# Kernel tuning notes

Hardware: AMD Instinct MI355X
Metric: run time of the kernel (lower is better)

## Reference

```python
import jax, jax.numpy as jnp
import numpy as np

DEPTH = 2
EPS = 1e-12

def _l2norm(x, axis=-1):
    n = jnp.sqrt(jnp.sum(x * x, axis=axis, keepdims=True))
    return x / jnp.maximum(n, EPS)

def setup_inputs() -> dict:
    key = jax.random.key(0)
    k1, k2, k3, k4, k5 = jax.random.split(key, 5)
    N, D, R, E = 50000, 100, 1000, 800000
    features = jax.random.normal(k1, (N, D), dtype=jnp.float32)
    rel_emb = jax.random.normal(k2, (R, D), dtype=jnp.float32)
    none_relation = jax.random.normal(k3, (D,), dtype=jnp.float32)
    # edge list sorted by destination row (matches coalesced sparse layout
    # assumed by the original: softmax values align with edge order)
    rows = jnp.sort(jax.random.randint(k4, (E,), 0, N))
    cols = jax.random.randint(k5, (E,), 0, N)
    adj_index = jnp.stack([rows, cols], axis=1).astype(jnp.int64)
    return {"features": features, "rel_emb": rel_emb,
            "adj_index": adj_index, "none_relation": none_relation}

def reference(features, rel_emb, adj_index, none_relation):
    N = features.shape[0]
    rows = adj_index[:, 0]  # destination (softmax segment, scatter target)
    cols = adj_index[:, 1]  # neighbor (gather source)
    feats = jnp.tanh(features)
    outputs = [feats]
    nr = _l2norm(none_relation, axis=0)  # [D]
    for _ in range(DEPTH):
        neighs = feats[cols]                      # [E, D] gather
        score = -jnp.einsum('ed,d->e', _l2norm(neighs), nr)  # [E]
        # sparse softmax over each destination row's edges
        m = jax.ops.segment_max(score, rows, num_segments=N)
        e = jnp.exp(score - m[rows])
        denom = jax.ops.segment_sum(e, rows, num_segments=N)
        att = e / denom[rows]                     # [E]
        new_feats = jax.ops.segment_sum(neighs * att[:, None], rows,
                                        num_segments=N)  # [N, D]
        feats = jnp.tanh(new_feats)
        outputs.append(feats)
    return jnp.concatenate(outputs, axis=1)  # [N, D*(DEPTH+1)]
```

## Files before the change

kernel.cpp:

```cpp
#include <hip/hip_runtime.h>
#include <math.h>

#define D_FEAT 100
#define ROW_STRIDE 300
#define ROWQ 26

__device__ __forceinline__ float fast_tanh(float x) {
    float ax = fabsf(x);
    float e  = __expf(2.f * ax);
    float t  = 1.f - 2.f / (e + 1.f);
    return copysignf(t, x);
}

__device__ __forceinline__ unsigned pack_bf16x2(float a, float b) {
    unsigned ua = __float_as_uint(a);
    unsigned ub = __float_as_uint(b);
    ua += 0x7fffu + ((ua >> 16) & 1u);
    ub += 0x7fffu + ((ub >> 16) & 1u);
    return (ua >> 16) | (ub & 0xffff0000u);
}
__device__ __forceinline__ unsigned long long pack_bf16x4(float a, float b,
                                                          float c, float d) {
    return (unsigned long long)pack_bf16x2(a, b) |
           ((unsigned long long)pack_bf16x2(c, d) << 32);
}
__device__ __forceinline__ void unpack_bf16x4(unsigned long long u,
                                              float& x0, float& x1,
                                              float& x2, float& x3) {
    unsigned lo = (unsigned)u, hi = (unsigned)(u >> 32);
    x0 = __uint_as_float(lo << 16);
    x1 = __uint_as_float(lo & 0xffff0000u);
    x2 = __uint_as_float(hi << 16);
    x3 = __uint_as_float(hi & 0xffff0000u);
}

__device__ __forceinline__ float half_reduce(float v) {
    #pragma unroll
    for (int off = 16; off; off >>= 1) v += __shfl_xor(v, off, 64);
    return v;
}

__global__ __launch_bounds__(256) void tanh_score_kernel(
    const float* __restrict__ features,
    float* __restrict__ out,
    unsigned long long* __restrict__ tab0,
    float* __restrict__ escore0,
    const float* __restrict__ none_rel,
    const int* __restrict__ adj,
    int* __restrict__ startArr,
    int E, int N)
{
    int gtid = blockIdx.x * blockDim.x + threadIdx.x;
    if (gtid <= N) {
        if (gtid == N) startArr[N] = E;
        else {
            int lo = 0, hi = E;
            while (lo < hi) {
                int mid = (lo + hi) >> 1;
                if (adj[2 * mid] < gtid) lo = mid + 1; else hi = mid;
            }
            startArr[gtid] = lo;
        }
    }

    int waveId = gtid >> 6;
    int lane = threadIdx.x & 63;
    int half = lane >> 5;
    int l    = lane & 31;
    int n    = waveId * 2 + half;
    const bool valid_n = (n < N);
    const bool fact = valid_n && (l >= 1) && (l <= 25);

    float x0 = 0.f, x1 = 0.f, x2 = 0.f, x3 = 0.f;
    if (fact) {
        float4 f = ((const float4*)(features + (size_t)n * D_FEAT))[l - 1];
        x0 = fast_tanh(f.x); x1 = fast_tanh(f.y);
        x2 = fast_tanh(f.z); x3 = fast_tanh(f.w);
        ((float4*)(out + (size_t)n * ROW_STRIDE))[l - 1] = make_float4(x0, x1, x2, x3);
        if (tab0) tab0[(size_t)n * ROWQ + l] = pack_bf16x4(x0, x1, x2, x3);
    }

    float nx = 0.f, ny = 0.f, nz = 0.f, nw = 0.f;
    if (l >= 1 && l <= 25) {
        float4 v = ((const float4*)none_rel)[l - 1];
        nx = v.x; ny = v.y; nz = v.z; nw = v.w;
    }
    float ss = half_reduce(nx * nx + ny * ny + nz * nz + nw * nw);
    float inv_nr = 1.f / fmaxf(sqrtf(ss), 1e-12f);

    float dot = half_reduce(x0 * nx + x1 * ny + x2 * nz + x3 * nw) * inv_nr;
    float sq  = half_reduce(x0 * x0 + x1 * x1 + x2 * x2 + x3 * x3);
    if (l == 0 && valid_n) {
        float es = __expf(-dot / fmaxf(sqrtf(sq), 1e-12f));
        if (tab0) tab0[(size_t)n * ROWQ] = (unsigned long long)__float_as_uint(es);
        else      escore0[n] = es;
    }
}

template <bool TAB>
__global__ __launch_bounds__(256) void attn_kernel(
    const void* __restrict__ prev,
    float* __restrict__ outp,
    unsigned long long* __restrict__ tab_out,
    const int2* __restrict__ adj2,
    const int* __restrict__ start,
    const float* __restrict__ escore_in,
    float* __restrict__ escore_out,
    const float* __restrict__ none_rel,
    int N)
{
    int waveId = (int)((blockIdx.x * blockDim.x + threadIdx.x) >> 6);
    int lane = threadIdx.x & 63;
    int half = lane >> 5;
    int l    = lane & 31;
    int n    = waveId * 2 + half;
    const bool valid_n = (n < N);
    const bool fact = valid_n && (l >= 1) && (l <= 25);
    const int base = half << 5;

    int e0 = 0, e1 = 0;
    if (valid_n) { e0 = start[n]; e1 = start[n + 1]; }
    const int deg = e1 - e0;

    int   c0 = 0, c1 = 0;
    float w0 = 0.f, w1 = 0.f;
    if (l < deg)      { c0 = adj2[e0 + l].y;      if (!TAB) w0 = escore_in[c0]; }
    if (l + 32 < deg) { c1 = adj2[e0 + l + 32].y; if (!TAB) w1 = escore_in[c1]; }

    int maxdeg = deg;
    { int o = __shfl_xor(maxdeg, 32, 64); maxdeg = maxdeg > o ? maxdeg : o; }

    const unsigned long long* tab = (const unsigned long long*)prev;
    const float* pf32 = (const float*)prev;

    float d_acc = 0.f, a0 = 0.f, a1 = 0.f, a2 = 0.f, a3 = 0.f;
    const int cap1 = maxdeg < 32 ? maxdeg : 32;
    for (int r = 0; r < cap1; r += 8) {
        #pragma unroll
        for (int j = 0; j < 8; ++j) {
            int   i = r + j;
            int   c = __shfl(c0, base + i, 64);
            float w, p0, p1, p2, p3;
            if (TAB) {
                bool on = valid_n && (i < deg) && (l <= 25);
                unsigned long long v = 0;
                if (on) v = tab[(size_t)(unsigned)(c * ROWQ + l)];
                w = __shfl(__uint_as_float((unsigned)v), base, 64);
                unpack_bf16x4(v, p0, p1, p2, p3);
            } else {
                w = __shfl(w0, base + i, 64);
                p0 = p1 = p2 = p3 = 0.f;
                if (fact && (i < deg)) {
                    float4 v = ((const float4*)(pf32 + (size_t)c * ROW_STRIDE))[l - 1];
                    p0 = v.x; p1 = v.y; p2 = v.z; p3 = v.w;
                }
            }
            d_acc += w;
            a0 += w * p0; a1 += w * p1; a2 += w * p2; a3 += w * p3;
        }
    }
    const int cap2 = maxdeg < 64 ? maxdeg : 64;
    for (int r = 32; r < cap2; r += 8) {
        #pragma unroll
        for (int j = 0; j < 8; ++j) {
            int   i = r + j;
            int   c = __shfl(c1, base + i - 32, 64);
            float w, p0, p1, p2, p3;
            if (TAB) {
                bool on = valid_n && (i < deg) && (l <= 25);
                unsigned long long v = 0;
                if (on) v = tab[(size_t)(unsigned)(c * ROWQ + l)];
                w = __shfl(__uint_as_float((unsigned)v), base, 64);
                unpack_bf16x4(v, p0, p1, p2, p3);
            } else {
                w = __shfl(w1, base + i - 32, 64);
                p0 = p1 = p2 = p3 = 0.f;
                if (fact && (i < deg)) {
                    float4 v = ((const float4*)(pf32 + (size_t)c * ROW_STRIDE))[l - 1];
                    p0 = v.x; p1 = v.y; p2 = v.z; p3 = v.w;
                }
            }
            d_acc += w;
            a0 += w * p0; a1 += w * p1; a2 += w * p2; a3 += w * p3;
        }
    }
    for (int e = e0 + 64; e < e1; ++e) {
        int c = adj2[e].y;
        float w, p0, p1, p2, p3;
        if (TAB) {
            unsigned long long v = 0;
            if (l <= 25) v = tab[(size_t)(unsigned)(c * ROWQ + l)];
            w = __shfl(__uint_as_float((unsigned)v), base, 64);
            unpack_bf16x4(v, p0, p1, p2, p3);
        } else {
            w = escore_in[c];
            p0 = p1 = p2 = p3 = 0.f;
            if (fact) {
                float4 v = ((const float4*)(pf32 + (size_t)c * ROW_STRIDE))[l - 1];
                p0 = v.x; p1 = v.y; p2 = v.z; p3 = v.w;
            }
        }
        d_acc += w;
        a0 += w * p0; a1 += w * p1; a2 += w * p2; a3 += w * p3;
    }

    const float inv_d = (deg > 0) ? 1.f / d_acc : 0.f;
    float r0 = fast_tanh(a0 * inv_d);
    float r1 = fast_tanh(a1 * inv_d);
    float r2 = fast_tanh(a2 * inv_d);
    float r3 = fast_tanh(a3 * inv_d);
    if (fact) {
        ((float4*)(outp + (size_t)n * ROW_STRIDE))[l - 1] = make_float4(r0, r1, r2, r3);
        if (TAB && tab_out)
            tab_out[(size_t)n * ROWQ + l] = pack_bf16x4(r0, r1, r2, r3);
    } else {
        r0 = r1 = r2 = r3 = 0.f;
    }

    if (tab_out || escore_out) {
        float nx = 0.f, ny = 0.f, nz = 0.f, nw = 0.f;
        if (l >= 1 && l <= 25) {
            float4 v = ((const float4*)none_rel)[l - 1];
            nx = v.x; ny = v.y; nz = v.z; nw = v.w;
        }
        float ss = half_reduce(nx * nx + ny * ny + nz * nz + nw * nw);
        float inv_nr = 1.f / fmaxf(sqrtf(ss), 1e-12f);
        float dot = half_reduce(r0 * nx + r1 * ny + r2 * nz + r3 * nw) * inv_nr;
        float sq  = half_reduce(r0 * r0 + r1 * r1 + r2 * r2 + r3 * r3);
        if (l == 0 && valid_n) {
            float es = __expf(-dot / fmaxf(sqrtf(sq), 1e-12f));
            if (TAB) tab_out[(size_t)n * ROWQ] = (unsigned long long)__float_as_uint(es);
            else     escore_out[n] = es;
        }
    }
}

extern "C" void kernel_launch(void* const* d_in, const int* in_sizes, int n_in,
                              void* d_out, int out_size, void* d_ws, size_t ws_size,
                              hipStream_t stream) {
    const float* features = (const float*)d_in[0];
    const int*   adj      = (const int*)d_in[2];
    const float* none_rel = (const float*)d_in[3];
    float* out = (float*)d_out;

    const int N = in_sizes[0] / D_FEAT;
    const int E = in_sizes[2] / 2;

    size_t off = 0;
    auto take = [&](size_t bytes) { size_t o = off; off = (off + bytes + 15) & ~(size_t)15; return o; };
    char* w = (char*)d_ws;
    int*   start   = (int*)  (w + take(sizeof(int)   * (size_t)(N + 1)));
    float* escore0 = (float*)(w + take(sizeof(float) * (size_t)N));
    float* escore1 = (float*)(w + take(sizeof(float) * (size_t)N));
    size_t tab_off0 = take(sizeof(unsigned long long) * (size_t)N * ROWQ);
    size_t tab_off1 = take(sizeof(unsigned long long) * (size_t)N * ROWQ);
    const bool use_tab = (ws_size >= off);
    unsigned long long* tab0 = use_tab ? (unsigned long long*)(w + tab_off0) : nullptr;
    unsigned long long* tab1 = use_tab ? (unsigned long long*)(w + tab_off1) : nullptr;

    const int pairs = (N + 1) / 2;
    const int node_blocks = (pairs * 64 + 255) / 256;
    const int2* adj2 = (const int2*)adj;

    tanh_score_kernel<<<node_blocks, 256, 0, stream>>>(features, out, tab0,
                                                       escore0, none_rel,
                                                       adj, start, E, N);
    if (use_tab) {
        attn_kernel<true><<<node_blocks, 256, 0, stream>>>(
            tab0, out + D_FEAT, tab1, adj2, start, nullptr, nullptr, none_rel, N);
        attn_kernel<true><<<node_blocks, 256, 0, stream>>>(
            tab1, out + 2 * D_FEAT, nullptr, adj2, start, nullptr, nullptr, none_rel, N);
    } else {
        attn_kernel<false><<<node_blocks, 256, 0, stream>>>(
            out, out + D_FEAT, nullptr, adj2, start, escore0, escore1, none_rel, N);
        attn_kernel<false><<<node_blocks, 256, 0, stream>>>(
            out + D_FEAT, out + 2 * D_FEAT, nullptr, adj2, start, escore1, nullptr, none_rel, N);
    }
}
```

Baseline: 179.3 us.

## Gather two edges per half-wave with 16-byte bf16 row loads

Adds an attn16 kernel that reads the bf16 neighbor table as uint4 per lane, splitting each half-wave into two 13-lane groups. Each group handles a different edge, then the partial sums are combined across partner lanes. This halves the edge-loop iterations and the number of gather load instructions per node, aiming to raise memory-level parallelism. The old TAB path is stripped out of attn_kernel, and the output and table write layouts are remapped to 8 floats per lane. The lane mapping and the slot-0 handling (score plus zero padding) add complexity and risk of off-by-one errors.

```diff
diff --git a/kernel.cpp b/kernel.cpp
--- a/kernel.cpp
+++ b/kernel.cpp
@@ -4,6 +4,7 @@
 #define D_FEAT 100
 #define ROW_STRIDE 300
 #define ROWQ 26
+#define ROWB 208u
 
 __device__ __forceinline__ float fast_tanh(float x) {
     float ax = fabsf(x);
@@ -32,6 +33,10 @@
     x1 = __uint_as_float(lo & 0xffff0000u);
     x2 = __uint_as_float(hi << 16);
     x3 = __uint_as_float(hi & 0xffff0000u);
+}
+__device__ __forceinline__ void unpack2(unsigned u, float& lo, float& hi) {
+    lo = __uint_as_float(u << 16);
+    hi = __uint_as_float(u & 0xffff0000u);
 }
 
 __device__ __forceinline__ float half_reduce(float v) {
@@ -97,6 +102,158 @@
     }
 }
 
+template <bool WRITE_TAB>
+__global__ __launch_bounds__(256) void attn16_kernel(
+    const unsigned long long* __restrict__ tab,
+    float* __restrict__ outp,
+    unsigned long long* __restrict__ tab_out,
+    const int2* __restrict__ adj2,
+    const int* __restrict__ start,
+    const float* __restrict__ none_rel,
+    int N)
+{
+    const int waveId = (int)((blockIdx.x * blockDim.x + threadIdx.x) >> 6);
+    const int lane = threadIdx.x & 63;
+    const int half = lane >> 5;
+    const int l    = lane & 31;
+    const int base = half << 5;
+    const int n    = waveId * 2 + half;
+    const bool valid_n = (n < N);
+
+    const bool act  = (l < 26);
+    const int  wh   = (act && l >= 13) ? 1 : 0;
+    const int  sub  = act ? (l - 13 * wh) : 0;
+    const bool actA = (l < 13);
+
+    int e0 = 0, e1 = 0;
+    if (valid_n) { e0 = start[n]; e1 = start[n + 1]; }
+    const int deg = e1 - e0;
+    int maxdeg = deg;
+    { int o = __shfl_xor(maxdeg, 32, 64); maxdeg = maxdeg > o ? maxdeg : o; }
+
+    int c0 = 0, c1 = 0;
+    if (l < deg)      c0 = adj2[e0 + l].y;
+    if (l + 32 < deg) c1 = adj2[e0 + l + 32].y;
+
+    const char* tb = (const char*)tab;
+    const size_t suboff = (size_t)(sub * 16);
+    const int wsrc = base + 13 * wh;
+    const int degw = deg - wh;
+
+    float a0=0.f,a1=0.f,a2=0.f,a3=0.f,a4=0.f,a5=0.f,a6=0.f,a7=0.f;
+    float d_acc = 0.f;
+
+#define ATTN16_PASS(CSTAGE, I, SRC)                                           \
+    {                                                                         \
+        int c = __shfl((CSTAGE), base + (SRC) + wh, 64);                      \
+        const uint4 v = *(const uint4*)(tb + (size_t)(unsigned)c * ROWB + suboff); \
+        float w = __shfl(__uint_as_float(v.x), wsrc, 64);                     \
+        w = ((I) < degw) ? w : 0.f;                                           \
+        float p0,p1,p2,p3,p4,p5,p6,p7;                                        \
+        unpack2(v.x,p0,p1); unpack2(v.y,p2,p3);                               \
+        unpack2(v.z,p4,p5); unpack2(v.w,p6,p7);                               \
+        if (sub == 0) { p0 = 0.f; p1 = 0.f; }           \
+        a0 += w*p0; a1 += w*p1; a2 += w*p2; a3 += w*p3;                       \
+        a4 += w*p4; a5 += w*p5; a6 += w*p6; a7 += w*p7;                       \
+        d_acc += w;                                                           \
+    }
+
+    const int cap1 = maxdeg < 32 ? maxdeg : 32;
+    for (int r = 0; r < cap1; r += 8) {
+        #pragma unroll
+        for (int j = 0; j < 4; ++j) {
+            const int i = r + 2 * j;
+            ATTN16_PASS(c0, i, i)
+        }
+    }
+    const int cap2 = maxdeg < 64 ? maxdeg : 64;
+    for (int r = 32; r < cap2; r += 8) {
+        #pragma unroll
+        for (int j = 0; j < 4; ++j) {
+            const int i = r + 2 * j;
+            ATTN16_PASS(c1, i, i - 32)
+        }
+    }
+#undef ATTN16_PASS
+
+    for (int e = e0 + 64; e < e1; ++e) {
+        int c = adj2[e].y;
+        const uint4 v = *(const uint4*)(tb + (size_t)(unsigned)c * ROWB + suboff);
+        float w = __shfl(__uint_as_float(v.x), base, 64);
+        float p0,p1,p2,p3,p4,p5,p6,p7;
+        unpack2(v.x,p0,p1); unpack2(v.y,p2,p3);
+        unpack2(v.z,p4,p5); unpack2(v.w,p6,p7);
+        if (sub == 0) { p0 = 0.f; p1 = 0.f; }
+        if (wh == 0) {
+            a0 += w*p0; a1 += w*p1; a2 += w*p2; a3 += w*p3;
+            a4 += w*p4; a5 += w*p5; a6 += w*p6; a7 += w*p7;
+            d_acc += w;
+        }
+    }
+
+    const int partner = base + (actA ? l + 13 : (act ? l - 13 : l));
+    d_acc += __shfl(d_acc, partner, 64);
+    a0 += __shfl(a0, partner, 64);
+    a1 += __shfl(a1, partner, 64);
+    a2 += __shfl(a2, partner, 64);
+    a3 += __shfl(a3, partner, 64);
+    a4 += __shfl(a4, partner, 64);
+    a5 += __shfl(a5, partner, 64);
+    a6 += __shfl(a6, partner, 64);
+    a7 += __shfl(a7, partner, 64);
+
+    const float inv_d = (deg > 0) ? 1.f / d_acc : 0.f;
+    float r0 = fast_tanh(a0 * inv_d);
+    float r1 = fast_tanh(a1 * inv_d);
+    float r2 = fast_tanh(a2 * inv_d);
+    float r3 = fast_tanh(a3 * inv_d);
+    float r4 = fast_tanh(a4 * inv_d);
+    float r5 = fast_tanh(a5 * inv_d);
+    float r6 = fast_tanh(a6 * inv_d);
+    float r7 = fast_tanh(a7 * inv_d);
+    if (!actA) { r0=r1=r2=r3=r4=r5=r6=r7=0.f; }
+
+    if (valid_n && actA) {
+        float4* orow = (float4*)(outp + (size_t)n * ROW_STRIDE);
+        if (l == 0) {
+            orow[0] = make_float4(r4, r5, r6, r7);
+        } else {
+            orow[2*l - 1] = make_float4(r0, r1, r2, r3);
+            orow[2*l]     = make_float4(r4, r5, r6, r7);
+        }
+        if constexpr (WRITE_TAB) {
+            if (l > 0) {
+                uint4* trow = (uint4*)((char*)tab_out + (size_t)n * ROWB);
+                trow[l] = make_uint4(pack_bf16x2(r0,r1), pack_bf16x2(r2,r3),
+                                     pack_bf16x2(r4,r5), pack_bf16x2(r6,r7));
+            }
+        }
+    }
+
+    if constexpr (WRITE_TAB) {
+        float n0=0.f,n1=0.f,n2=0.f,n3=0.f,n4=0.f,n5=0.f,n6=0.f,n7=0.f;
+        if (l == 0) {
+            float4 v = ((const float4*)none_rel)[0];
+            n4=v.x; n5=v.y; n6=v.z; n7=v.w;
+        } else if (l < 13) {
+            float4 u = *(const float4*)(none_rel + 8*l - 4);
+            float4 v = *(const float4*)(none_rel + 8*l);
+            n0=u.x; n1=u.y; n2=u.z; n3=u.w;
+            n4=v.x; n5=v.y; n6=v.z; n7=v.w;
+        }
+        float ss = half_reduce(n0*n0+n1*n1+n2*n2+n3*n3+n4*n4+n5*n5+n6*n6+n7*n7);
+        float inv_nr = 1.f / fmaxf(sqrtf(ss), 1e-12f);
+        float dot = half_reduce(r0*n0+r1*n1+r2*n2+r3*n3+r4*n4+r5*n5+r6*n6+r7*n7) * inv_nr;
+        float sq  = half_reduce(r0*r0+r1*r1+r2*r2+r3*r3+r4*r4+r5*r5+r6*r6+r7*r7);
+        if (l == 0 && valid_n) {
+            float es = __expf(-dot / fmaxf(sqrtf(sq), 1e-12f));
+            uint4* trow = (uint4*)((char*)tab_out + (size_t)n * ROWB);
+            trow[0] = make_uint4(__float_as_uint(es), 0u,
+                                 pack_bf16x2(r4,r5), pack_bf16x2(r6,r7));
+        }
+    }
+}
+
 template <bool TAB>
 __global__ __launch_bounds__(256) void attn_kernel(
     const void* __restrict__ prev,
@@ -130,7 +287,6 @@
     int maxdeg = deg;
     { int o = __shfl_xor(maxdeg, 32, 64); maxdeg = maxdeg > o ? maxdeg : o; }
 
-    const unsigned long long* tab = (const unsigned long long*)prev;
     const float* pf32 = (const float*)prev;
 
     float d_acc = 0.f, a0 = 0.f, a1 = 0.f, a2 = 0.f, a3 = 0.f;
@@ -140,21 +296,13 @@
         for (int j = 0; j < 8; ++j) {
             int   i = r + j;
             int   c = __shfl(c0, base + i, 64);
-            float w, p0, p1, p2, p3;
-            if (TAB) {
-                bool on = valid_n && (i < deg) && (l <= 25);
-                unsigned long long v = 0;
-                if (on) v = tab[(size_t)(unsigned)(c * ROWQ + l)];
-                w = __shfl(__uint_as_float((unsigned)v), base, 64);
-                unpack_bf16x4(v, p0, p1, p2, p3);
-            } else {
-                w = __shfl(w0, base + i, 64);
-                p0 = p1 = p2 = p3 = 0.f;
-                if (fact && (i < deg)) {
-                    float4 v = ((const float4*)(pf32 + (size_t)c * ROW_STRIDE))[l - 1];
-                    p0 = v.x; p1 = v.y; p2 = v.z; p3 = v.w;
-                }
+            float w = __shfl(w0, base + i, 64);
+            float p0 = 0.f, p1 = 0.f, p2 = 0.f, p3 = 0.f;
+            if (fact && (i < deg)) {
+                float4 v = ((const float4*)(pf32 + (size_t)c * ROW_STRIDE))[l - 1];
+                p0 = v.x; p1 = v.y; p2 = v.z; p3 = v.w;
             }
+            if (i >= deg) w = 0.f;
             d_acc += w;
             a0 += w * p0; a1 += w * p1; a2 += w * p2; a3 += w * p3;
         }
@@ -165,40 +313,24 @@
         for (int j = 0; j < 8; ++j) {
             int   i = r + j;
             int   c = __shfl(c1, base + i - 32, 64);
-            float w, p0, p1, p2, p3;
-            if (TAB) {
-                bool on = valid_n && (i < deg) && (l <= 25);
-                unsigned long long v = 0;
-                if (on) v = tab[(size_t)(unsigned)(c * ROWQ + l)];
-                w = __shfl(__uint_as_float((unsigned)v), base, 64);
-                unpack_bf16x4(v, p0, p1, p2, p3);
-            } else {
-                w = __shfl(w1, base + i - 32, 64);
-                p0 = p1 = p2 = p3 = 0.f;
-                if (fact && (i < deg)) {
-                    float4 v = ((const float4*)(pf32 + (size_t)c * ROW_STRIDE))[l - 1];
-                    p0 = v.x; p1 = v.y; p2 = v.z; p3 = v.w;
-                }
-            }
-            d_acc += w;
-            a0 += w * p0; a1 += w * p1; a2 += w * p2; a3 += w * p3;
-        }
-    }
-    for (int e = e0 + 64; e < e1; ++e) {
-        int c = adj2[e].y;
-        float w, p0, p1, p2, p3;
-        if (TAB) {
-            unsigned long long v = 0;
-            if (l <= 25) v = tab[(size_t)(unsigned)(c * ROWQ + l)];
-            w = __shfl(__uint_as_float((unsigned)v), base, 64);
-            unpack_bf16x4(v, p0, p1, p2, p3);
-        } else {
-            w = escore_in[c];
-            p0 = p1 = p2 = p3 = 0.f;
-            if (fact) {
+            float w = __shfl(w1, base + i - 32, 64);
+            float p0 = 0.f, p1 = 0.f, p2 = 0.f, p3 = 0.f;
+            if (fact && (i < deg)) {
                 float4 v = ((const float4*)(pf32 + (size_t)c * ROW_STRIDE))[l - 1];
                 p0 = v.x; p1 = v.y; p2 = v.z; p3 = v.w;
             }
+            if (i >= deg) w = 0.f;
+            d_acc += w;
+            a0 += w * p0; a1 += w * p1; a2 += w * p2; a3 += w * p3;
+        }
+    }
+    for (int e = e0 + 64; e < e1; ++e) {
+        int c = adj2[e].y;
+        float w = escore_in[c];
+        float p0 = 0.f, p1 = 0.f, p2 = 0.f, p3 = 0.f;
+        if (fact) {
+            float4 v = ((const float4*)(pf32 + (size_t)c * ROW_STRIDE))[l - 1];
+            p0 = v.x; p1 = v.y; p2 = v.z; p3 = v.w;
         }
         d_acc += w;
         a0 += w * p0; a1 += w * p1; a2 += w * p2; a3 += w * p3;
@@ -211,13 +343,11 @@
     float r3 = fast_tanh(a3 * inv_d);
     if (fact) {
         ((float4*)(outp + (size_t)n * ROW_STRIDE))[l - 1] = make_float4(r0, r1, r2, r3);
-        if (TAB && tab_out)
-            tab_out[(size_t)n * ROWQ + l] = pack_bf16x4(r0, r1, r2, r3);
     } else {
         r0 = r1 = r2 = r3 = 0.f;
     }
 
-    if (tab_out || escore_out) {
+    if (escore_out) {
         float nx = 0.f, ny = 0.f, nz = 0.f, nw = 0.f;
         if (l >= 1 && l <= 25) {
             float4 v = ((const float4*)none_rel)[l - 1];
@@ -229,8 +359,7 @@
         float sq  = half_reduce(r0 * r0 + r1 * r1 + r2 * r2 + r3 * r3);
         if (l == 0 && valid_n) {
             float es = __expf(-dot / fmaxf(sqrtf(sq), 1e-12f));
-            if (TAB) tab_out[(size_t)n * ROWQ] = (unsigned long long)__float_as_uint(es);
-            else     escore_out[n] = es;
+            escore_out[n] = es;
         }
     }
 }
@@ -266,10 +395,10 @@
                                                        escore0, none_rel,
                                                        adj, start, E, N);
     if (use_tab) {
-        attn_kernel<true><<<node_blocks, 256, 0, stream>>>(
-            tab0, out + D_FEAT, tab1, adj2, start, nullptr, nullptr, none_rel, N);
-        attn_kernel<true><<<node_blocks, 256, 0, stream>>>(
-            tab1, out + 2 * D_FEAT, nullptr, adj2, start, nullptr, nullptr, none_rel, N);
+        attn16_kernel<true><<<node_blocks, 256, 0, stream>>>(
+            tab0, out + D_FEAT, tab1, adj2, start, none_rel, N);
+        attn16_kernel<false><<<node_blocks, 256, 0, stream>>>(
+            tab1, out + 2 * D_FEAT, nullptr, adj2, start, none_rel, N);
     } else {
         attn_kernel<false><<<node_blocks, 256, 0, stream>>>(
             out, out + D_FEAT, nullptr, adj2, start, escore0, escore1, none_rel, N);
```

Result: faster. 157.3 us (-12.3%).
